# Performance work log

Measured on AMD Instinct MI355X. Metric: run time of the kernel, lower is better.

Reference implementation:

```python
import jax, jax.numpy as jnp
import numpy as np

B, T, A, C = 8, 256, 2, 128
R, H, OUT = 128, 128, 256  # readin_dim, session_embed_size, out_count


def _uni(k, shape, fan_in):
    # matches torch kaiming_uniform_(a=sqrt(5)) / nn.Linear default: U(-1/sqrt(fan_in), 1/sqrt(fan_in))
    b = 1.0 / np.sqrt(fan_in)
    return jax.random.uniform(k, shape, jnp.float32, -b, b)


def setup_inputs() -> dict:
    key = jax.random.key(0)
    ks = jax.random.split(key, 16)
    return {
        "state_in": jax.random.normal(ks[0], (B, T, A, C), jnp.float32),
        "session": jax.random.normal(ks[1], (B, H), jnp.float32),
        "subject": jax.random.normal(ks[2], (B, H), jnp.float32),
        "array": jax.random.normal(ks[3], (B, A, H), jnp.float32),
        "query": jax.random.normal(ks[4], (R,), jnp.float32),
        "pos_embeds": _uni(ks[5], (C, R), R),
        # key_project: Linear(R+H, R) -> GELU -> Linear(R, R); weights stored [in, out]
        "kW1": _uni(ks[6], (R + H, R), R + H), "kb1": _uni(ks[7], (R,), R + H),
        "kW2": _uni(ks[8], (R, R), R), "kb2": _uni(ks[9], (R,), R),
        # value_project: Linear(1+R+H, R) -> GELU -> Linear(R, OUT)
        # concat order in forward is [pos_embed (R), session (H), state_in (1)]
        "vW1": _uni(ks[10], (R + H + 1, R), R + H + 1), "vb1": _uni(ks[11], (R,), R + H + 1),
        "vW2": _uni(ks[12], (R, OUT), R), "vb2": _uni(ks[13], (OUT,), R),
    }


def reference(state_in, session, subject, array, query, pos_embeds,
              kW1, kb1, kW2, kb2, vW1, vb1, vW2, vb2):
    r = pos_embeds.shape[-1]
    h = session.shape[-1]
    scale = jnp.sqrt(jnp.asarray(r, state_in.dtype))
    # keys: cat([pos (c,r) expand b, session (b,h) expand c]) -> MLP. Decompose the
    # first Linear over the concat blocks (same math, no expanded concat buffer).
    kh = (pos_embeds @ kW1[:r])[None, :, :] + (session @ kW1[r:])[:, None, :] + kb1  # [b,c,r]
    keys = jax.nn.gelu(kh, approximate=False) @ kW2 + kb2                           # [b,c,r]
    # values: cat([pos, session, state_in]) over (b,t,a,c) -> MLP, decomposed likewise
    vh = ((pos_embeds @ vW1[:r])[None, None, None, :, :]
          + (session @ vW1[r:r + h])[:, None, None, None, :]
          + state_in[..., None] * vW1[r + h]
          + vb1)                                                                     # [b,t,a,c,r]
    values = jax.nn.gelu(vh, approximate=False) @ vW2 + vb2                          # [b,t,a,c,out]
    scores = jnp.einsum('bcr,r->bc', keys, query) / scale
    w = jax.nn.softmax(scores, axis=-1)                                              # [b,c]
    return jnp.einsum('bc,btach->btah', w, values)                                   # [b,t,a,out]
```

## Files before the change

### kernel.cpp

```cpp
#include <hip/hip_runtime.h>
#include <math.h>

#define B_ 8
#define T_ 256
#define A_ 2
#define C_ 128
#define R_ 128
#define H_ 128
#define OUT_ 256

#define WS_PCK 0
#define WS_PCV 16384
#define WS_PSK 32768
#define WS_PSV 33792
#define WS_QK  34816
#define WS_WSM 34944
#define WS_W1  36864
#define WS_W2  167936
#define WS_W3  299008
#define WS_S0  430080
#define WS_TOTAL 431104

__device__ __forceinline__ float gelu_fast(float x) {
    const float ax = fabsf(x);
    float q = fmaf(ax, 0.019527f, 0.000343654f);
    q = fmaf(q, ax, 0.1151945f);
    q = fmaf(q, ax, 0.19685217f);
    q = fmaf(q, ax, 1.0f);
    const float r  = __builtin_amdgcn_rcpf(q);
    const float r2 = r * r;
    const float r4 = r2 * r2;
    return fmaf(-0.5f * ax, r4, fmaxf(x, 0.0f));
}

__global__ __launch_bounds__(256) void prep_kernel(
    const float* __restrict__ session,
    const float* __restrict__ query,
    const float* __restrict__ pos,
    const float* __restrict__ kW1,
    const float* __restrict__ kb1,
    const float* __restrict__ kW2,
    const float* __restrict__ vW1,
    const float* __restrict__ vb1,
    float* __restrict__ ws)
{
    const int g = blockIdx.x * 256 + threadIdx.x;
    if (g < 16384) {
        const int c = g >> 7, r = g & 127;
        float acc = 0.0f;
        #pragma unroll 16
        for (int k = 0; k < R_; ++k)
            acc += pos[c * R_ + k] * kW1[k * R_ + r];
        ws[WS_PCK + g] = acc;
    } else if (g < 32768) {
        const int e = g - 16384;
        const int c = e >> 7, r = e & 127;
        float acc = 0.0f;
        #pragma unroll 16
        for (int k = 0; k < R_; ++k)
            acc += pos[c * R_ + k] * vW1[k * R_ + r];
        ws[WS_PCV + e] = acc;
    } else if (g < 33792) {
        const int e = g - 32768;
        const int b = e >> 7, r = e & 127;
        float acc = kb1[r];
        #pragma unroll 16
        for (int k = 0; k < H_; ++k)
            acc += session[b * H_ + k] * kW1[(R_ + k) * R_ + r];
        ws[WS_PSK + e] = acc;
    } else if (g < 34816) {
        const int e = g - 33792;
        const int b = e >> 7, r = e & 127;
        float acc = vb1[r];
        #pragma unroll 16
        for (int k = 0; k < H_; ++k)
            acc += session[b * H_ + k] * vW1[(R_ + k) * R_ + r];
        ws[WS_PSV + e] = acc;
    } else if (g < 34944) {
        const int r = g - 34816;
        float acc = 0.0f;
        #pragma unroll 16
        for (int j = 0; j < R_; ++j)
            acc += kW2[r * R_ + j] * query[j];
        ws[WS_QK + r] = acc;
    } else if (g < 35968) {
        ws[WS_S0 + (g - 34944)] = 0.0f;
    }
}

__global__ __launch_bounds__(1024) void softmax_kernel(float* __restrict__ ws)
{
    __shared__ float pskL[R_];
    __shared__ float qkL[R_];
    __shared__ float part8[8][C_];
    __shared__ float sc[C_];
    __shared__ float red[C_];

    const int b   = blockIdx.x;
    const int tid = threadIdx.x;
    const int q   = tid >> 7;
    const int c   = tid & 127;

    if (tid < 128) {
        pskL[tid] = ws[WS_PSK + b * R_ + tid];
        qkL[tid]  = ws[WS_QK + tid];
    }
    __syncthreads();

    const float* __restrict__ pckc = ws + WS_PCK + c * R_ + q * 16;
    float acc = 0.0f;
    #pragma unroll
    for (int i = 0; i < 16; ++i) {
        const float x = pckc[i] + pskL[q * 16 + i];
        acc += gelu_fast(x) * qkL[q * 16 + i];
    }
    part8[q][c] = acc;
    __syncthreads();

    if (tid < 128) {
        float s = part8[0][tid];
        #pragma unroll
        for (int j = 1; j < 8; ++j) s += part8[j][tid];
        s *= 0.08838834764831845f;
        sc[tid]  = s;
        red[tid] = s;
    }
    __syncthreads();
    for (int st = 64; st > 0; st >>= 1) {
        if (tid < st) red[tid] = fmaxf(red[tid], red[tid + st]);
        __syncthreads();
    }
    const float m = red[0];
    __syncthreads();
    if (tid < 128) {
        const float e = __expf(sc[tid] - m);
        sc[tid]  = e;
        red[tid] = e;
    }
    __syncthreads();
    for (int st = 64; st > 0; st >>= 1) {
        if (tid < st) red[tid] += red[tid + st];
        __syncthreads();
    }
    if (tid < 128) ws[WS_WSM + b * C_ + tid] = sc[tid] / red[0];
}

__global__ __launch_bounds__(256) void coef_kernel(
    const float* __restrict__ vW1,
    float* __restrict__ ws)
{
    __shared__ float s0sh[R_];

    const int blk = blockIdx.x;
    const int b   = blk >> 6;
    const int cp  = blk & 63;
    const int tid = threadIdx.x;
    const int c   = cp * 2 + (tid >> 7);
    const int r   = tid & 127;

    const float vr  = vW1[(R_ + H_) * R_ + r];
    const float vr2 = vr * vr;
    const float vr3 = vr2 * vr;
    const float cc  = ws[WS_PCV + c * R_ + r] + ws[WS_PSV + b * R_ + r];
    const float wgt = ws[WS_WSM + b * C_ + c];

    const float ax = fabsf(cc);
    float qq = fmaf(ax, 0.019527f, 0.000343654f);
    qq = fmaf(qq, ax, 0.1151945f);
    qq = fmaf(qq, ax, 0.19685217f);
    qq = fmaf(qq, ax, 1.0f);
    const float qi  = __builtin_amdgcn_rcpf(qq);
    const float qi2 = qi * qi;
    const float h   = 0.5f * qi2 * qi2;
    const float Phi = (cc >= 0.0f) ? (1.0f - h) : h;
    const float cc2 = cc * cc;
    const float phi = 0.3989422804f * __expf(-0.5f * cc2);
    const float g0 = cc * Phi;
    const float g1 = fmaf(cc, phi, Phi);
    const float g2 = 0.5f * phi * (2.0f - cc2);
    const float g3 = phi * cc * (cc2 - 4.0f) * (1.0f / 6.0f);

    const size_t idx = (size_t)(b * C_ + c) * R_ + r;
    ws[WS_W1 + idx] = wgt * g1 * vr;
    ws[WS_W2 + idx] = wgt * g2 * vr2;
    ws[WS_W3 + idx] = wgt * g3 * vr3;

    const float contrib = wgt * g0;
    if (tid >= 128) s0sh[r] = contrib;
    __syncthreads();
    if (tid < 128) atomicAdd(ws + WS_S0 + b * R_ + r, contrib + s0sh[r]);
}

__global__ __launch_bounds__(512) void main_kernel(
    const float* __restrict__ state,
    const float* __restrict__ vW2,
    const float* __restrict__ vb2,
    const float* __restrict__ ws,
    float* __restrict__ out)
{
    __shared__ __align__(16) float sv[16 * C_];
    __shared__ float4 smem[4][8][R_];
    __shared__ float4 p4[4][R_];

    const int blk = blockIdx.x;
    const int b   = blk >> 5;
    const int grp = blk & 31;
    const int tid = threadIdx.x;
    const int rh  = tid >> 8;
    const int t2  = tid & 255;
    const int k   = t2 & 31;
    const int seg = t2 >> 5;
    const int r0  = k * 4;

    const float* __restrict__ srow = state + (size_t)(b * 512 + grp * 16) * C_;
    #pragma unroll
    for (int i = 0; i < 4; ++i) sv[tid + 512 * i] = srow[tid + 512 * i];
    __syncthreads();

    const size_t pbase = (size_t)(b * C_) * R_ + r0;
    const float* __restrict__ W1p = ws + WS_W1 + pbase;
    const float* __restrict__ W2p = ws + WS_W2 + pbase;
    const float* __restrict__ W3p = ws + WS_W3 + pbase;

    float4 a[8];
    #pragma unroll
    for (int j = 0; j < 8; ++j) a[j] = make_float4(0.f, 0.f, 0.f, 0.f);

    const int cbeg = seg * 16;
    const int rbase = rh * 8;
    #pragma unroll 2
    for (int i = 0; i < 16; ++i) {
        const int c = cbeg + i;
        const float4 w1 = *(const float4*)(W1p + (size_t)c * R_);
        const float4 w2 = *(const float4*)(W2p + (size_t)c * R_);
        const float4 w3 = *(const float4*)(W3p + (size_t)c * R_);
        #pragma unroll
        for (int j = 0; j < 8; ++j) {
            const float s  = sv[(rbase + j) * C_ + c];
            const float s2 = s * s;
            const float s3 = s2 * s;
            a[j].x = fmaf(w1.x, s, a[j].x); a[j].x = fmaf(w2.x, s2, a[j].x); a[j].x = fmaf(w3.x, s3, a[j].x);
            a[j].y = fmaf(w1.y, s, a[j].y); a[j].y = fmaf(w2.y, s2, a[j].y); a[j].y = fmaf(w3.y, s3, a[j].y);
            a[j].z = fmaf(w1.z, s, a[j].z); a[j].z = fmaf(w2.z, s2, a[j].z); a[j].z = fmaf(w3.z, s3, a[j].z);
            a[j].w = fmaf(w1.w, s, a[j].w); a[j].w = fmaf(w2.w, s2, a[j].w); a[j].w = fmaf(w3.w, s3, a[j].w);
        }
    }

    smem[rh * 2 + 0][seg][r0 + 0] = make_float4(a[0].x, a[1].x, a[2].x, a[3].x);
    smem[rh * 2 + 0][seg][r0 + 1] = make_float4(a[0].y, a[1].y, a[2].y, a[3].y);
    smem[rh * 2 + 0][seg][r0 + 2] = make_float4(a[0].z, a[1].z, a[2].z, a[3].z);
    smem[rh * 2 + 0][seg][r0 + 3] = make_float4(a[0].w, a[1].w, a[2].w, a[3].w);
    smem[rh * 2 + 1][seg][r0 + 0] = make_float4(a[4].x, a[5].x, a[6].x, a[7].x);
    smem[rh * 2 + 1][seg][r0 + 1] = make_float4(a[4].y, a[5].y, a[6].y, a[7].y);
    smem[rh * 2 + 1][seg][r0 + 2] = make_float4(a[4].z, a[5].z, a[6].z, a[7].z);
    smem[rh * 2 + 1][seg][r0 + 3] = make_float4(a[4].w, a[5].w, a[6].w, a[7].w);
    __syncthreads();

    {
        const int qd = tid >> 7;
        const int rr = tid & 127;
        float4 v = smem[qd][0][rr];
        #pragma unroll
        for (int sg = 1; sg < 8; ++sg) {
            const float4 t = smem[qd][sg][rr];
            v.x += t.x; v.y += t.y; v.z += t.z; v.w += t.w;
        }
        const float s0v = ws[WS_S0 + b * R_ + rr];
        v.x += s0v; v.y += s0v; v.z += s0v; v.w += s0v;
        p4[qd][rr] = v;
    }
    __syncthreads();

    float4 (*ep)[16][64] = (float4 (*)[16][64])smem;
    const int hq  = tid & 63;
    const int kq  = (tid >> 6) & 3;
    const int erh = tid >> 8;
    const int h0  = hq * 4;

    float4 o[8];
    #pragma unroll
    for (int j = 0; j < 8; ++j) o[j] = make_float4(0.f, 0.f, 0.f, 0.f);
    const int rrb = kq * 32;
    #pragma unroll 4
    for (int i = 0; i < 32; ++i) {
        const int rr = rrb + i;
        const float4 plo = p4[erh * 2 + 0][rr];
        const float4 phi = p4[erh * 2 + 1][rr];
        const float4 wv4 = *(const float4*)(vW2 + rr * OUT_ + h0);
        o[0].x = fmaf(plo.x, wv4.x, o[0].x); o[0].y = fmaf(plo.x, wv4.y, o[0].y);
        o[0].z = fmaf(plo.x, wv4.z, o[0].z); o[0].w = fmaf(plo.x, wv4.w, o[0].w);
        o[1].x = fmaf(plo.y, wv4.x, o[1].x); o[1].y = fmaf(plo.y, wv4.y, o[1].y);
        o[1].z = fmaf(plo.y, wv4.z, o[1].z); o[1].w = fmaf(plo.y, wv4.w, o[1].w);
        o[2].x = fmaf(plo.z, wv4.x, o[2].x); o[2].y = fmaf(plo.z, wv4.y, o[2].y);
        o[2].z = fmaf(plo.z, wv4.z, o[2].z); o[2].w = fmaf(plo.z, wv4.w, o[2].w);
        o[3].x = fmaf(plo.w, wv4.x, o[3].x); o[3].y = fmaf(plo.w, wv4.y, o[3].y);
        o[3].z = fmaf(plo.w, wv4.z, o[3].z); o[3].w = fmaf(plo.w, wv4.w, o[3].w);
        o[4].x = fmaf(phi.x, wv4.x, o[4].x); o[4].y = fmaf(phi.x, wv4.y, o[4].y);
        o[4].z = fmaf(phi.x, wv4.z, o[4].z); o[4].w = fmaf(phi.x, wv4.w, o[4].w);
        o[5].x = fmaf(phi.y, wv4.x, o[5].x); o[5].y = fmaf(phi.y, wv4.y, o[5].y);
        o[5].z = fmaf(phi.y, wv4.z, o[5].z); o[5].w = fmaf(phi.y, wv4.w, o[5].w);
        o[6].x = fmaf(phi.z, wv4.x, o[6].x); o[6].y = fmaf(phi.z, wv4.y, o[6].y);
        o[6].z = fmaf(phi.z, wv4.z, o[6].z); o[6].w = fmaf(phi.z, wv4.w, o[6].w);
        o[7].x = fmaf(phi.w, wv4.x, o[7].x); o[7].y = fmaf(phi.w, wv4.y, o[7].y);
        o[7].z = fmaf(phi.w, wv4.z, o[7].z); o[7].w = fmaf(phi.w, wv4.w, o[7].w);
    }
    #pragma unroll
    for (int j = 0; j < 8; ++j) ep[kq][erh * 8 + j][hq] = o[j];
    __syncthreads();

    const int row  = tid >> 5;
    const int hqa  = tid & 31;
    float* __restrict__ orow = out + (size_t)(b * 512 + grp * 16 + row) * OUT_;
    #pragma unroll
    for (int half = 0; half < 2; ++half) {
        const int hh = hqa + half * 32;
        const float4 e0 = ep[0][row][hh];
        const float4 e1 = ep[1][row][hh];
        const float4 e2 = ep[2][row][hh];
        const float4 e3 = ep[3][row][hh];
        const float4 bias = *(const float4*)(vb2 + hh * 4);
        float4 oo;
        oo.x = e0.x + e1.x + e2.x + e3.x + bias.x;
        oo.y = e0.y + e1.y + e2.y + e3.y + bias.y;
        oo.z = e0.z + e1.z + e2.z + e3.z + bias.z;
        oo.w = e0.w + e1.w + e2.w + e3.w + bias.w;
        *(float4*)(orow + hh * 4) = oo;
    }
}

extern "C" void kernel_launch(void* const* d_in, const int* in_sizes, int n_in,
                              void* d_out, int out_size, void* d_ws, size_t ws_size,
                              hipStream_t stream) {
    const float* state   = (const float*)d_in[0];
    const float* session = (const float*)d_in[1];
    const float* query   = (const float*)d_in[4];
    const float* pos     = (const float*)d_in[5];
    const float* kW1     = (const float*)d_in[6];
    const float* kb1     = (const float*)d_in[7];
    const float* kW2     = (const float*)d_in[8];
    const float* vW1     = (const float*)d_in[10];
    const float* vb1     = (const float*)d_in[11];
    const float* vW2     = (const float*)d_in[12];
    const float* vb2     = (const float*)d_in[13];

    float* ws  = (float*)d_ws;
    float* out = (float*)d_out;

    prep_kernel<<<141, 256, 0, stream>>>(session, query, pos, kW1, kb1, kW2,
                                         vW1, vb1, ws);
    softmax_kernel<<<B_, 1024, 0, stream>>>(ws);
    coef_kernel<<<512, 256, 0, stream>>>(vW1, ws);
    main_kernel<<<B_ * 32, 512, 0, stream>>>(state, vW2, vb2, ws, out);
}
```

Before: 106.1 us.

## Fuse softmax and coefficient kernels into main kernel, recomputing per block

Drops the separate softmax and coefficient kernels and folds both into the main kernel. Each block now recomputes the key scores and softmax with a wave shuffle reduction, then builds the polynomial coefficients chunk by chunk in shared memory instead of writing and reading three large global workspace arrays. This removes two launches, the global round trip of the coefficient tensors, and the atomic accumulation. In exchange, the softmax and GELU-coefficient work is repeated 32 times per batch, adds extra barriers, and raises shared memory use.

```diff
diff --git a/kernel.cpp b/kernel.cpp
--- a/kernel.cpp
+++ b/kernel.cpp
@@ -14,12 +14,10 @@
 #define WS_PSK 32768
 #define WS_PSV 33792
 #define WS_QK  34816
-#define WS_WSM 34944
-#define WS_W1  36864
-#define WS_W2  167936
-#define WS_W3  299008
-#define WS_S0  430080
-#define WS_TOTAL 431104
+#define WS_TOTAL 34944
+
+#define WL_OFF   12288
+#define PART_OFF 12416
 
 __device__ __forceinline__ float gelu_fast(float x) {
     const float ax = fabsf(x);
@@ -83,195 +81,166 @@
         for (int j = 0; j < R_; ++j)
             acc += kW2[r * R_ + j] * query[j];
         ws[WS_QK + r] = acc;
-    } else if (g < 35968) {
-        ws[WS_S0 + (g - 34944)] = 0.0f;
-    }
-}
-
-__global__ __launch_bounds__(1024) void softmax_kernel(float* __restrict__ ws)
-{
-    __shared__ float pskL[R_];
-    __shared__ float qkL[R_];
-    __shared__ float part8[8][C_];
-    __shared__ float sc[C_];
-    __shared__ float red[C_];
-
-    const int b   = blockIdx.x;
-    const int tid = threadIdx.x;
-    const int q   = tid >> 7;
-    const int c   = tid & 127;
-
-    if (tid < 128) {
-        pskL[tid] = ws[WS_PSK + b * R_ + tid];
-        qkL[tid]  = ws[WS_QK + tid];
-    }
-    __syncthreads();
-
-    const float* __restrict__ pckc = ws + WS_PCK + c * R_ + q * 16;
-    float acc = 0.0f;
-    #pragma unroll
-    for (int i = 0; i < 16; ++i) {
-        const float x = pckc[i] + pskL[q * 16 + i];
-        acc += gelu_fast(x) * qkL[q * 16 + i];
-    }
-    part8[q][c] = acc;
-    __syncthreads();
-
-    if (tid < 128) {
-        float s = part8[0][tid];
-        #pragma unroll
-        for (int j = 1; j < 8; ++j) s += part8[j][tid];
-        s *= 0.08838834764831845f;
-        sc[tid]  = s;
-        red[tid] = s;
-    }
-    __syncthreads();
-    for (int st = 64; st > 0; st >>= 1) {
-        if (tid < st) red[tid] = fmaxf(red[tid], red[tid + st]);
-        __syncthreads();
-    }
-    const float m = red[0];
-    __syncthreads();
-    if (tid < 128) {
-        const float e = __expf(sc[tid] - m);
-        sc[tid]  = e;
-        red[tid] = e;
-    }
-    __syncthreads();
-    for (int st = 64; st > 0; st >>= 1) {
-        if (tid < st) red[tid] += red[tid + st];
-        __syncthreads();
-    }
-    if (tid < 128) ws[WS_WSM + b * C_ + tid] = sc[tid] / red[0];
-}
-
-__global__ __launch_bounds__(256) void coef_kernel(
-    const float* __restrict__ vW1,
-    float* __restrict__ ws)
-{
-    __shared__ float s0sh[R_];
-
-    const int blk = blockIdx.x;
-    const int b   = blk >> 6;
-    const int cp  = blk & 63;
-    const int tid = threadIdx.x;
-    const int c   = cp * 2 + (tid >> 7);
-    const int r   = tid & 127;
-
-    const float vr  = vW1[(R_ + H_) * R_ + r];
-    const float vr2 = vr * vr;
-    const float vr3 = vr2 * vr;
-    const float cc  = ws[WS_PCV + c * R_ + r] + ws[WS_PSV + b * R_ + r];
-    const float wgt = ws[WS_WSM + b * C_ + c];
-
-    const float ax = fabsf(cc);
-    float qq = fmaf(ax, 0.019527f, 0.000343654f);
-    qq = fmaf(qq, ax, 0.1151945f);
-    qq = fmaf(qq, ax, 0.19685217f);
-    qq = fmaf(qq, ax, 1.0f);
-    const float qi  = __builtin_amdgcn_rcpf(qq);
-    const float qi2 = qi * qi;
-    const float h   = 0.5f * qi2 * qi2;
-    const float Phi = (cc >= 0.0f) ? (1.0f - h) : h;
-    const float cc2 = cc * cc;
-    const float phi = 0.3989422804f * __expf(-0.5f * cc2);
-    const float g0 = cc * Phi;
-    const float g1 = fmaf(cc, phi, Phi);
-    const float g2 = 0.5f * phi * (2.0f - cc2);
-    const float g3 = phi * cc * (cc2 - 4.0f) * (1.0f / 6.0f);
-
-    const size_t idx = (size_t)(b * C_ + c) * R_ + r;
-    ws[WS_W1 + idx] = wgt * g1 * vr;
-    ws[WS_W2 + idx] = wgt * g2 * vr2;
-    ws[WS_W3 + idx] = wgt * g3 * vr3;
-
-    const float contrib = wgt * g0;
-    if (tid >= 128) s0sh[r] = contrib;
-    __syncthreads();
-    if (tid < 128) atomicAdd(ws + WS_S0 + b * R_ + r, contrib + s0sh[r]);
+    }
 }
 
 __global__ __launch_bounds__(512) void main_kernel(
     const float* __restrict__ state,
+    const float* __restrict__ vW1,
     const float* __restrict__ vW2,
     const float* __restrict__ vb2,
     const float* __restrict__ ws,
     float* __restrict__ out)
 {
     __shared__ __align__(16) float sv[16 * C_];
-    __shared__ float4 smem[4][8][R_];
+    __shared__ __align__(16) float U[16384];
     __shared__ float4 p4[4][R_];
 
     const int blk = blockIdx.x;
     const int b   = blk >> 5;
     const int grp = blk & 31;
     const int tid = threadIdx.x;
-    const int rh  = tid >> 8;
-    const int t2  = tid & 255;
-    const int k   = t2 & 31;
-    const int seg = t2 >> 5;
-    const int r0  = k * 4;
 
     const float* __restrict__ srow = state + (size_t)(b * 512 + grp * 16) * C_;
     #pragma unroll
     for (int i = 0; i < 4; ++i) sv[tid + 512 * i] = srow[tid + 512 * i];
-    __syncthreads();
-
-    const size_t pbase = (size_t)(b * C_) * R_ + r0;
-    const float* __restrict__ W1p = ws + WS_W1 + pbase;
-    const float* __restrict__ W2p = ws + WS_W2 + pbase;
-    const float* __restrict__ W3p = ws + WS_W3 + pbase;
+
+    {
+        const int c  = tid >> 2;
+        const int rs = tid & 3;
+        const float4* __restrict__ pk4 = (const float4*)(ws + WS_PCK + c * R_ + rs * 32);
+        const float4* __restrict__ ps4 = (const float4*)(ws + WS_PSK + b * R_ + rs * 32);
+        const float4* __restrict__ qk4 = (const float4*)(ws + WS_QK + rs * 32);
+        float acc = 0.0f;
+        #pragma unroll
+        for (int i = 0; i < 8; ++i) {
+            const float4 pk = pk4[i];
+            const float4 ps = ps4[i];
+            const float4 qq = qk4[i];
+            acc += gelu_fast(pk.x + ps.x) * qq.x;
+            acc += gelu_fast(pk.y + ps.y) * qq.y;
+            acc += gelu_fast(pk.z + ps.z) * qq.z;
+            acc += gelu_fast(pk.w + ps.w) * qq.w;
+        }
+        U[PART_OFF + c * 4 + rs] = acc;
+    }
+    __syncthreads();
+
+    if (tid < 64) {
+        const float4 pa = *(const float4*)&U[PART_OFF + tid * 8];
+        const float4 pb = *(const float4*)&U[PART_OFF + tid * 8 + 4];
+        float s0 = (pa.x + pa.y + pa.z + pa.w) * 0.08838834764831845f;
+        float s1 = (pb.x + pb.y + pb.z + pb.w) * 0.08838834764831845f;
+        float m = fmaxf(s0, s1);
+        #pragma unroll
+        for (int off = 32; off > 0; off >>= 1) m = fmaxf(m, __shfl_xor(m, off));
+        const float e0 = __expf(s0 - m);
+        const float e1 = __expf(s1 - m);
+        float sum = e0 + e1;
+        #pragma unroll
+        for (int off = 32; off > 0; off >>= 1) sum += __shfl_xor(sum, off);
+        U[WL_OFF + tid * 2 + 0] = e0 / sum;
+        U[WL_OFF + tid * 2 + 1] = e1 / sum;
+    }
+    __syncthreads();
+
+    const int rcoef = tid & 127;
+    const int cg    = tid >> 7;
+    const float vr   = vW1[(R_ + H_) * R_ + rcoef];
+    const float vr2  = vr * vr;
+    const float vr3  = vr2 * vr;
+    const float psvr = ws[WS_PSV + b * R_ + rcoef];
+
+    const int rh    = tid >> 8;
+    const int t2    = tid & 255;
+    const int k     = t2 & 31;
+    const int seg   = t2 >> 5;
+    const int r0    = k * 4;
+    const int rbase = rh * 8;
 
     float4 a[8];
     #pragma unroll
     for (int j = 0; j < 8; ++j) a[j] = make_float4(0.f, 0.f, 0.f, 0.f);
-
-    const int cbeg = seg * 16;
-    const int rbase = rh * 8;
-    #pragma unroll 2
-    for (int i = 0; i < 16; ++i) {
-        const int c = cbeg + i;
-        const float4 w1 = *(const float4*)(W1p + (size_t)c * R_);
-        const float4 w2 = *(const float4*)(W2p + (size_t)c * R_);
-        const float4 w3 = *(const float4*)(W3p + (size_t)c * R_);
+    float s0reg = 0.0f;
+
+    for (int chunk = 0; chunk < 4; ++chunk) {
         #pragma unroll
         for (int j = 0; j < 8; ++j) {
-            const float s  = sv[(rbase + j) * C_ + c];
-            const float s2 = s * s;
-            const float s3 = s2 * s;
-            a[j].x = fmaf(w1.x, s, a[j].x); a[j].x = fmaf(w2.x, s2, a[j].x); a[j].x = fmaf(w3.x, s3, a[j].x);
-            a[j].y = fmaf(w1.y, s, a[j].y); a[j].y = fmaf(w2.y, s2, a[j].y); a[j].y = fmaf(w3.y, s3, a[j].y);
-            a[j].z = fmaf(w1.z, s, a[j].z); a[j].z = fmaf(w2.z, s2, a[j].z); a[j].z = fmaf(w3.z, s3, a[j].z);
-            a[j].w = fmaf(w1.w, s, a[j].w); a[j].w = fmaf(w2.w, s2, a[j].w); a[j].w = fmaf(w3.w, s3, a[j].w);
+            const int cl = cg * 8 + j;
+            const int c  = chunk * 32 + cl;
+            const float cc  = ws[WS_PCV + c * R_ + rcoef] + psvr;
+            const float wgt = U[WL_OFF + c];
+            const float ax = fabsf(cc);
+            float qq = fmaf(ax, 0.019527f, 0.000343654f);
+            qq = fmaf(qq, ax, 0.1151945f);
+            qq = fmaf(qq, ax, 0.19685217f);
+            qq = fmaf(qq, ax, 1.0f);
+            const float qi  = __builtin_amdgcn_rcpf(qq);
+            const float qi2 = qi * qi;
+            const float hh  = 0.5f * qi2 * qi2;
+            const float Phi = (cc >= 0.0f) ? (1.0f - hh) : hh;
+            const float cc2 = cc * cc;
+            const float phi = 0.3989422804f * __expf(-0.5f * cc2);
+            const float g0 = cc * Phi;
+            const float g1 = fmaf(cc, phi, Phi);
+            const float g2 = 0.5f * phi * (2.0f - cc2);
+            const float g3 = phi * cc * (cc2 - 4.0f) * (1.0f / 6.0f);
+            U[       cl * R_ + rcoef] = wgt * g1 * vr;
+            U[4096 + cl * R_ + rcoef] = wgt * g2 * vr2;
+            U[8192 + cl * R_ + rcoef] = wgt * g3 * vr3;
+            s0reg += wgt * g0;
         }
-    }
-
-    smem[rh * 2 + 0][seg][r0 + 0] = make_float4(a[0].x, a[1].x, a[2].x, a[3].x);
-    smem[rh * 2 + 0][seg][r0 + 1] = make_float4(a[0].y, a[1].y, a[2].y, a[3].y);
-    smem[rh * 2 + 0][seg][r0 + 2] = make_float4(a[0].z, a[1].z, a[2].z, a[3].z);
-    smem[rh * 2 + 0][seg][r0 + 3] = make_float4(a[0].w, a[1].w, a[2].w, a[3].w);
-    smem[rh * 2 + 1][seg][r0 + 0] = make_float4(a[4].x, a[5].x, a[6].x, a[7].x);
-    smem[rh * 2 + 1][seg][r0 + 1] = make_float4(a[4].y, a[5].y, a[6].y, a[7].y);
-    smem[rh * 2 + 1][seg][r0 + 2] = make_float4(a[4].z, a[5].z, a[6].z, a[7].z);
-    smem[rh * 2 + 1][seg][r0 + 3] = make_float4(a[4].w, a[5].w, a[6].w, a[7].w);
+        __syncthreads();
+
+        #pragma unroll
+        for (int i = 0; i < 4; ++i) {
+            const int cl = seg * 4 + i;
+            const int c  = chunk * 32 + cl;
+            const float4 w1 = *(const float4*)&U[       cl * R_ + r0];
+            const float4 w2 = *(const float4*)&U[4096 + cl * R_ + r0];
+            const float4 w3 = *(const float4*)&U[8192 + cl * R_ + r0];
+            #pragma unroll
+            for (int j = 0; j < 8; ++j) {
+                const float s  = sv[(rbase + j) * C_ + c];
+                const float s2 = s * s;
+                const float s3 = s2 * s;
+                a[j].x = fmaf(w1.x, s, a[j].x); a[j].x = fmaf(w2.x, s2, a[j].x); a[j].x = fmaf(w3.x, s3, a[j].x);
+                a[j].y = fmaf(w1.y, s, a[j].y); a[j].y = fmaf(w2.y, s2, a[j].y); a[j].y = fmaf(w3.y, s3, a[j].y);
+                a[j].z = fmaf(w1.z, s, a[j].z); a[j].z = fmaf(w2.z, s2, a[j].z); a[j].z = fmaf(w3.z, s3, a[j].z);
+                a[j].w = fmaf(w1.w, s, a[j].w); a[j].w = fmaf(w2.w, s2, a[j].w); a[j].w = fmaf(w3.w, s3, a[j].w);
+            }
+        }
+        __syncthreads();
+    }
+
+    float4 (*tp)[8][R_] = (float4 (*)[8][R_])U;
+    tp[rh * 2 + 0][seg][r0 + 0] = make_float4(a[0].x, a[1].x, a[2].x, a[3].x);
+    tp[rh * 2 + 0][seg][r0 + 1] = make_float4(a[0].y, a[1].y, a[2].y, a[3].y);
+    tp[rh * 2 + 0][seg][r0 + 2] = make_float4(a[0].z, a[1].z, a[2].z, a[3].z);
+    tp[rh * 2 + 0][seg][r0 + 3] = make_float4(a[0].w, a[1].w, a[2].w, a[3].w);
+    tp[rh * 2 + 1][seg][r0 + 0] = make_float4(a[4].x, a[5].x, a[6].x, a[7].x);
+    tp[rh * 2 + 1][seg][r0 + 1] = make_float4(a[4].y, a[5].y, a[6].y, a[7].y);
+    tp[rh * 2 + 1][seg][r0 + 2] = make_float4(a[4].z, a[5].z, a[6].z, a[7].z);
+    tp[rh * 2 + 1][seg][r0 + 3] = make_float4(a[4].w, a[5].w, a[6].w, a[7].w);
+    sv[cg * R_ + rcoef] = s0reg;
     __syncthreads();
 
     {
         const int qd = tid >> 7;
         const int rr = tid & 127;
-        float4 v = smem[qd][0][rr];
+        float4 v = tp[qd][0][rr];
         #pragma unroll
         for (int sg = 1; sg < 8; ++sg) {
-            const float4 t = smem[qd][sg][rr];
+            const float4 t = tp[qd][sg][rr];
             v.x += t.x; v.y += t.y; v.z += t.z; v.w += t.w;
         }
-        const float s0v = ws[WS_S0 + b * R_ + rr];
+        const float s0v = sv[rr] + sv[R_ + rr] + sv[2 * R_ + rr] + sv[3 * R_ + rr];
         v.x += s0v; v.y += s0v; v.z += s0v; v.w += s0v;
         p4[qd][rr] = v;
     }
     __syncthreads();
 
-    float4 (*ep)[16][64] = (float4 (*)[16][64])smem;
+    float4 (*ep)[16][64] = (float4 (*)[16][64])U;
     const int hq  = tid & 63;
     const int kq  = (tid >> 6) & 3;
     const int erh = tid >> 8;
@@ -346,9 +315,7 @@
     float* ws  = (float*)d_ws;
     float* out = (float*)d_out;
 
-    prep_kernel<<<141, 256, 0, stream>>>(session, query, pos, kW1, kb1, kW2,
+    prep_kernel<<<137, 256, 0, stream>>>(session, query, pos, kW1, kb1, kW2,
                                          vW1, vb1, ws);
-    softmax_kernel<<<B_, 1024, 0, stream>>>(ws);
-    coef_kernel<<<512, 256, 0, stream>>>(vW1, ws);
-    main_kernel<<<B_ * 32, 512, 0, stream>>>(state, vW2, vb2, ws, out);
+    main_kernel<<<B_ * 32, 512, 0, stream>>>(state, vW1, vW2, vb2, ws, out);
 }
```

Result: slower. 108.9 us (+2.7%).
